# Kernel optimization log

Hardware: AMD Instinct MI355X
Metric: run time of the kernel (lower is better)

Reference implementation:

```python
import jax, jax.numpy as jnp
import numpy as np

N = 16384          # batch of signals
DIM_T = 256        # time steps per signal
DT = 0.01          # integration dt (intg_lev=1 -> dt_intg = dt)
NUF = 256          # num_units_feat
HID_XI = 128       # hidlayers_xi
HID_AUX = 64       # hidlayers_aux1_dec
LEN_INTG = DIM_T   # (dim_t-1)*intg_lev + 1 with intg_lev=1


def _linear_init(key, fan_in, fan_out):
    # torch nn.Linear default: U(-1/sqrt(fan_in), 1/sqrt(fan_in))
    s = 1.0 / np.sqrt(fan_in)
    kw, kb = jax.random.split(key)
    W = jax.random.uniform(kw, (fan_in, fan_out), minval=-s, maxval=s, dtype=jnp.float32)
    b = jax.random.uniform(kb, (fan_out,), minval=-s, maxval=s, dtype=jnp.float32)
    return W, b


def setup_inputs() -> dict:
    key = jax.random.key(0)
    ks = jax.random.split(key, 12)
    data = jax.random.normal(ks[0], (N, DIM_T), dtype=jnp.float32)
    omega = jax.random.normal(ks[1], (N, 1), dtype=jnp.float32)
    eps = jax.random.normal(ks[2], (N, 1), dtype=jnp.float32)
    # feature extractor (mlp branch): [dim_t+1 -> 256 -> 256], relu after both (actfun_output=True)
    W_feat1, b_feat1 = _linear_init(ks[3], DIM_T + 1, NUF)
    W_feat2, b_feat2 = _linear_init(ks[4], NUF, NUF)
    # xi mean head: MLP [256 -> 128 -> 1] then Softplus
    W_xim1, b_xim1 = _linear_init(ks[5], NUF, HID_XI)
    W_xim2, b_xim2 = _linear_init(ks[6], HID_XI, 1)
    # xi lnvar head: MLP [256 -> 128 -> 1]
    W_xil1, b_xil1 = _linear_init(ks[7], NUF, HID_XI)
    W_xil2, b_xil2 = _linear_init(ks[8], HID_XI, 1)
    # decoder aux1 MLP: [dim_z_aux1+1=2 -> 64 -> 1]
    W_aux1, b_aux1 = _linear_init(ks[9], 2, HID_AUX)
    W_aux2, b_aux2 = _linear_init(ks[10], HID_AUX, 1)
    return dict(data=data, omega=omega, eps=eps,
                W_feat1=W_feat1, b_feat1=b_feat1, W_feat2=W_feat2, b_feat2=b_feat2,
                W_xim1=W_xim1, b_xim1=b_xim1, W_xim2=W_xim2, b_xim2=b_xim2,
                W_xil1=W_xil1, b_xil1=b_xil1, W_xil2=W_xil2, b_xil2=b_xil2,
                W_aux1=W_aux1, b_aux1=b_aux1, W_aux2=W_aux2, b_aux2=b_aux2)


def reference(data, omega, eps,
              W_feat1, b_feat1, W_feat2, b_feat2,
              W_xim1, b_xim1, W_xim2, b_xim2,
              W_xil1, b_xil1, W_xil2, b_xil2,
              W_aux1, b_aux1, W_aux2, b_aux2):
    relu = jax.nn.relu
    # ---- encode_xi ----
    x_ = jnp.concatenate([data, omega], axis=1)                 # [n, dim_t+1]
    feat = relu(relu(x_ @ W_feat1 + b_feat1) @ W_feat2 + b_feat2)  # [n, 256]
    xi_mean = jax.nn.softplus(relu(feat @ W_xim1 + b_xim1) @ W_xim2 + b_xim2)  # [n, 1]
    xi_lnvar = relu(feat @ W_xil1 + b_xil1) @ W_xil2 + b_xil2                  # [n, 1]
    # ---- draw (reparameterization + clamp to feasible range [0, 1]) ----
    xi = xi_mean + jnp.exp(0.5 * xi_lnvar) * eps
    xi = jnp.clip(xi, 0.0, 1.0)
    # ---- decode: Euler odeint over LEN_INTG steps of state yy=[y, dy/dt] ----
    init_y = data[:, :1]                                        # [n, 1]
    initcond = jnp.concatenate([init_y, jnp.zeros_like(init_y)], axis=1)  # [n, 2]

    def step(yy, _):
        # physics: d[y, v]/dt = [v, 0]; aux MLP adds acceleration from (z_aux1=omega, y)
        aux_in = jnp.concatenate([omega, yy[:, :1]], axis=1)    # [n, 2]
        acc = relu(aux_in @ W_aux1 + b_aux1) @ W_aux2 + b_aux2  # [n, 1]
        dyy = jnp.concatenate([yy[:, 1:2], acc], axis=1)        # [n, 2]
        return yy + DT * dyy, yy

    _, yy_seq = jax.lax.scan(step, initcond, None, length=LEN_INTG)  # [len_intg, n, 2]
    y_seq = yy_seq[:, :, 0].T                                   # [n, dim_t] (intg_lev=1)
    t_intg = DT * jnp.arange(LEN_INTG, dtype=jnp.float32)       # [dim_t]
    x_PAB = jnp.exp(-jnp.abs(xi) * t_intg[None, :]) * y_seq     # [n, dim_t]
    return xi_mean, xi_lnvar, x_PAB
```

## Files before the change

kernel.cpp:

```cpp
#include <hip/hip_runtime.h>
#include <math.h>

#define NROWS 16384
#define DT_C 0.01f

typedef short s16x8 __attribute__((ext_vector_type(8)));
typedef float f32x4 __attribute__((ext_vector_type(4)));
typedef float f32x2 __attribute__((ext_vector_type(2)));
typedef unsigned long long u64;
typedef unsigned long long u64x2 __attribute__((ext_vector_type(2)));

__device__ __forceinline__ unsigned short f2bf(float f) {
    unsigned u = __float_as_uint(f);
    u += 0x7fffu + ((u >> 16) & 1u);
    return (unsigned short)(u >> 16);
}
__device__ __forceinline__ unsigned pack2bf(float a, float b) {
    return (unsigned)f2bf(a) | ((unsigned)f2bf(b) << 16);
}
template <int CTRL>
__device__ __forceinline__ float dppadd(float v) {
    int x = __builtin_amdgcn_update_dpp(0, __float_as_int(v), CTRL, 0xF, 0xF, true);
    return v + __int_as_float(x);
}
__device__ __forceinline__ float sum16(float p) {
    p = dppadd<0xB1>(p);
    p = dppadd<0x4E>(p);
    p = dppadd<0x141>(p);
    p = dppadd<0x140>(p);
    return p;
}
__device__ __forceinline__ unsigned ordf(float f) {
    unsigned u = __float_as_uint(f);
    return u ^ ((unsigned)((int)u >> 31) | 0x80000000u);
}

__global__ __launch_bounds__(256) void prep_k(
    const float* __restrict__ Wf1, const float* __restrict__ Wf2,
    const float* __restrict__ Wm1, const float* __restrict__ Wl1,
    const float* __restrict__ bm1, const float* __restrict__ bl1,
    unsigned short* __restrict__ wpack, float* __restrict__ biasH)
{
    const int id = blockIdx.x * 256 + threadIdx.x;
    const int n  = id & 255;
    const int k8 = (id >> 8) & 31;
    const int s  = id >> 13;

    unsigned short tmp[8];
    #pragma unroll
    for (int j = 0; j < 8; ++j) {
        const int k = k8 * 8 + j;
        float v;
        if (s == 0)      v = Wf1[k * 256 + n];
        else if (s == 1) v = Wf2[k * 256 + n];
        else             v = (n < 128) ? Wm1[k * 128 + n] : Wl1[k * 128 + n - 128];
        tmp[j] = f2bf(v);
    }
    *(uint4*)&wpack[((s * 32 + k8) * 256 + n) * 8] = *(const uint4*)tmp;

    if (id < 256) biasH[id] = (id < 128) ? bm1[id] : bl1[id - 128];
}

__global__ __launch_bounds__(512, 4) void fused_k(
    const float* __restrict__ data, const float* __restrict__ omega,
    const float* __restrict__ eps_g,
    const unsigned short* __restrict__ wpack, const float* __restrict__ biasH,
    const float* __restrict__ bf1, const float* __restrict__ bf2,
    const float* __restrict__ w256g,
    const float* __restrict__ Wm2, const float* __restrict__ bm2,
    const float* __restrict__ Wl2, const float* __restrict__ bl2,
    const float* __restrict__ Wa1, const float* __restrict__ ba1,
    const float* __restrict__ Wa2, const float* __restrict__ ba2,
    float* __restrict__ out_mean, float* __restrict__ out_lnvar,
    float* __restrict__ xout)
{
    __shared__ __align__(16) unsigned char smem[59136];
    unsigned short* As1 = (unsigned short*)smem;
    unsigned short* Hs  = (unsigned short*)(smem + 16384);
    float* headsF = (float*)smem;
    float* omg = (float*)(smem + 32768);
    float* xiS = omg + 32;
    float* tS  = (float*)(smem + 33024);
    float* dP  = (float*)(smem + 41728);
    u64*  keyU = (u64*)(smem + 41728);

    const int tid  = threadIdx.x;
    const int wid  = tid >> 6;
    const int lane = tid & 63;
    const int ln   = lane & 15;
    const int quad = lane >> 4;
    const int r0   = blockIdx.x * 32;

    {
        #pragma unroll
        for (int g2 = 0; g2 < 4; ++g2) {
            const int unit = g2 * 512 + tid;
            const int m    = unit >> 6;
            const int c16  = unit & 63;
            const int kblk = c16 >> 1;
            const int h    = c16 & 1;
            const float4 v = *(const float4*)&data[(size_t)(r0 + m) * 256 + c16 * 4];
            unsigned* d = (unsigned*)&As1[((kblk * 32) + (m ^ (kblk & 7))) * 8 + h * 4];
            d[0] = pack2bf(v.x, v.y);
            d[1] = pack2bf(v.z, v.w);
        }
        if (tid < 32) omg[tid] = omega[r0 + tid];
    }

    const int sr = tid >> 4;
    const int sl = tid & 15;
    float tA[4], dAv[4], dBv[4];
    u64 key[4];
    float k0f, Af, Bf, y0_s;
    {
        const float om_s = omega[r0 + sr];
        y0_s = data[(size_t)(r0 + sr) * 256];
        const u64 ky0 = ((u64)ordf(y0_s)) << 6;
        float k0p = 0.f, Ap = 0.f, Bp = 0.f;
        #pragma unroll
        for (int m = 0; m < 4; ++m) {
            const int i = sl * 4 + m;
            const float a = fmaf(om_s, Wa1[i], ba1[i]);
            const float w = Wa1[64 + i];
            const float c = Wa2[i];
            const float ca = c * a, cw = c * w;
        const bool wpos = w > 0.f;
            tA[m]  = -a / w;
            dAv[m] = wpos ? ca : -ca;
            dBv[m] = wpos ? cw : -cw;
            key[m] = (((u64)ordf(tA[m])) << 6) | (u64)i;
            const bool crossed = key[m] < ky0;
            if (wpos == crossed) { Ap += ca; Bp += cw; }
            k0p += crossed ? 1.f : 0.f;
            keyU[sr * 66 + i] = key[m];
        }
        k0f = sum16(k0p);
        Af  = sum16(Ap) + ba2[0];
        Bf  = sum16(Bp);
    }
    __syncthreads();

    {
        int rk[4] = {0, 0, 0, 0};
        const u64* krow = keyU + sr * 66;
        for (int j = 0; j < 64; j += 2) {
            const u64x2 kk = *(const u64x2*)&krow[j];
            #pragma unroll
            for (int m = 0; m < 4; ++m)
                rk[m] += (int)(kk.x < key[m]) + (int)(kk.y < key[m]);
        }
        __syncthreads();
        #pragma unroll
        for (int m = 0; m < 4; ++m) {
            const int idx = sr * 68 + 2 + rk[m];
            tS[idx] = tA[m];
            *(f32x2*)&dP[2 * idx] = f32x2{dAv[m], dBv[m]};
        }
        if (sl == 0) {
            const int b = sr * 68;
            const float INFV = __builtin_inff();
            tS[b] = -INFV; tS[b + 1] = -INFV; tS[b + 66] = INFV; tS[b + 67] = INFV;
            const f32x2 z = {0.f, 0.f};
            *(f32x2*)&dP[2 * b] = z;          *(f32x2*)&dP[2 * (b + 1)] = z;
            *(f32x2*)&dP[2 * (b + 66)] = z;   *(f32x2*)&dP[2 * (b + 67)] = z;
        }
    }

    f32x4 acc[2][2];

    auto seed = [&](const float* bias) {
        #pragma unroll
        for (int nt = 0; nt < 2; ++nt) {
            const float b = bias[wid * 32 + nt * 16 + ln];
            acc[0][nt] = f32x4{b, b, b, b};
            acc[1][nt] = acc[0][nt];
        }
    };

    auto run_stage = [&](const unsigned short* Ap, const unsigned short* wp) {
        #pragma unroll
        for (int c = 0; c < 4; ++c) {
            #pragma unroll
            for (int kk = 0; kk < 2; ++kk) {
                const int kb   = kk * 4 + quad;
                const int kblk = c * 8 + kb;
                const int f    = kblk & 7;
                s16x8 b0 = *(const s16x8*)&wp[((size_t)(kblk * 256) + wid * 32 + 0 * 16 + ln) * 8];
                s16x8 b1 = *(const s16x8*)&wp[((size_t)(kblk * 256) + wid * 32 + 1 * 16 + ln) * 8];
                s16x8 a0 = *(const s16x8*)&Ap[(kblk * 32 + (ln ^ f)) * 8];
                s16x8 a1 = *(const s16x8*)&Ap[(kblk * 32 + ((ln ^ f) + 16)) * 8];
                acc[0][0] = __builtin_amdgcn_mfma_f32_16x16x32_bf16(a0, b0, acc[0][0], 0, 0, 0);
                acc[1][0] = __builtin_amdgcn_mfma_f32_16x16x32_bf16(a1, b0, acc[1][0], 0, 0, 0);
                acc[0][1] = __builtin_amdgcn_mfma_f32_16x16x32_bf16(a0, b1, acc[0][1], 0, 0, 0);
                acc[1][1] = __builtin_amdgcn_mfma_f32_16x16x32_bf16(a1, b1, acc[1][1], 0, 0, 0);
            }
        }
    };

    auto write_packed = [&](unsigned short* dst, bool addOm) {
        #pragma unroll
        for (int nt = 0; nt < 2; ++nt) {
            const int col = wid * 32 + nt * 16 + ln;
            const int kg  = col >> 3, f = kg & 7, jj = col & 7;
            const float wo = addOm ? w256g[col] : 0.f;
            #pragma unroll
            for (int mt = 0; mt < 2; ++mt) {
                #pragma unroll
                for (int r = 0; r < 4; ++r) {
                    const int row = mt * 16 + quad * 4 + r;
                    float v = acc[mt][nt][r];
                    if (addOm) v = fmaf(omg[row], wo, v);
                    v = fmaxf(v, 0.f);
                    dst[(kg * 32 + (row ^ f)) * 8 + jj] = f2bf(v);
                }
            }
        }
    };

    seed(bf1);
    run_stage(As1, wpack);
    write_packed(Hs, true);
    __syncthreads();
    seed(bf2);
    run_stage(Hs, wpack + 65536);
    write_packed(As1, false);
    __syncthreads();
    seed(biasH);
    run_stage(As1, wpack + 131072);
    __syncthreads();
    #pragma unroll
    for (int nt = 0; nt < 2; ++nt) {
        const int col = wid * 32 + nt * 16 + ln;
        #pragma unroll
        for (int mt = 0; mt < 2; ++mt) {
            #pragma unroll
            for (int r = 0; r < 4; ++r) {
                const int row = mt * 16 + quad * 4 + r;
                headsF[row * 256 + ((col + row * 8) & 255)] = fmaxf(acc[mt][nt][r], 0.f);
            }
        }
    }
    __syncthreads();

    {
        const int m = tid >> 4, l = tid & 15;
        float pm = 0.f, pl = 0.f;
        #pragma unroll
        for (int q = 0; q < 2; ++q) {
            const int c0 = l * 8 + q * 4;
            const float4 hm = *(const float4*)&headsF[m * 256 + ((c0 + m * 8) & 255)];
            const float4 wm = *(const float4*)&Wm2[c0];
            const float4 hl = *(const float4*)&headsF[m * 256 + ((128 + c0 + m * 8) & 255)];
            const float4 wl = *(const float4*)&Wl2[c0];
            pm = fmaf(hm.w, wm.w, fmaf(hm.z, wm.z, fmaf(hm.y, wm.y, fmaf(hm.x, wm.x, pm))));
            pl = fmaf(hl.w, wl.w, fmaf(hl.z, wl.z, fmaf(hl.y, wl.y, fmaf(hl.x, wl.x, pl))));
        }
        pm = sum16(pm);
        pl = sum16(pl);
        if (l == 0) {
            const float xm  = pm + bm2[0];
            const float mean = fmaxf(xm, 0.f) + log1pf(expf(-fabsf(xm)));
            const float lnv  = pl + bl2[0];
            out_mean[r0 + m]  = mean;
            out_lnvar[r0 + m] = lnv;
            float xi = mean + expf(0.5f * lnv) * eps_g[r0 + m];
            xiS[m] = fminf(fmaxf(xi, 0.f), 1.f);
        }
    }
    __syncthreads();

    if (sl == 0) {
        const float xi   = xiS[sr];
        const float dfac = expf(-xi * DT_C);
        const float* tSr = tS + sr * 68 + 2;
        const float* dPb = dP + (sr * 68 + 2) * 2;
        int   k    = (int)k0f;
        float segA = Af, segB = Bf;
        float tLo  = tSr[k - 1], tHi = tSr[k], tHi2 = tSr[k + 1], tLo2 = tSr[k - 2];
        f32x2 dU = *(const f32x2*)&dPb[2 * k];
        f32x2 dD = *(const f32x2*)&dPb[2 * (k - 1)];
        float ym = y0_s, yc = y0_s;
        float pr = fmaf(segB, y0_s, segA);
        float d  = 1.f;
        const float DT2 = DT_C * DT_C;
        float* orow = xout + (size_t)(r0 + sr) * 256;

        auto step = [&](float& dst) {
            if (__builtin_expect(yc >= tHi, 0)) {
                do {
                    segA += dU.x; segB += dU.y;
                    dD = dU;
                    tLo2 = tLo; tLo = tHi; tHi = tHi2;
                    ++k;
                    tHi2 = tSr[k + 1];
                    dU = *(const f32x2*)&dPb[2 * k];
                } while (yc >= tHi);
            } else if (__builtin_expect(yc < tLo, 0)) {
                do {
                    segA -= dD.x; segB -= dD.y;
                    dU = dD;
                    tHi2 = tHi; tHi = tLo; tLo = tLo2;
                    --k;
                    tLo2 = tSr[k - 2];
                    dD = *(const f32x2*)&dPb[2 * (k - 1)];
                } while (yc < tLo);
            }
            const float pn = fmaf(segB, yc, segA);
            dst = ym * d;
            d *= dfac;
            const float yn = fmaf(DT2, pr, fmaf(2.f, yc, -ym));
            ym = yc; yc = yn; pr = pn;
        };

        for (int g = 0; g < 64; ++g) {
            float4 cv;
            step(cv.x); step(cv.y); step(cv.z); step(cv.w);
            *(float4*)&orow[g * 4] = cv;
        }
    }
}

extern "C" void kernel_launch(void* const* d_in, const int* in_sizes, int n_in,
                              void* d_out, int out_size, void* d_ws, size_t ws_size,
                              hipStream_t stream)
{
    const float* data    = (const float*)d_in[0];
    const float* omega   = (const float*)d_in[1];
    const float* eps     = (const float*)d_in[2];
    const float* W_feat1 = (const float*)d_in[3];
    const float* b_feat1 = (const float*)d_in[4];
    const float* W_feat2 = (const float*)d_in[5];
    const float* b_feat2 = (const float*)d_in[6];
    const float* W_xim1  = (const float*)d_in[7];
    const float* b_xim1  = (const float*)d_in[8];
    const float* W_xim2  = (const float*)d_in[9];
    const float* b_xim2  = (const float*)d_in[10];
    const float* W_xil1  = (const float*)d_in[11];
    const float* b_xil1  = (const float*)d_in[12];
    const float* W_xil2  = (const float*)d_in[13];
    const float* b_xil2  = (const float*)d_in[14];
    const float* W_aux1  = (const float*)d_in[15];
    const float* b_aux1  = (const float*)d_in[16];
    const float* W_aux2  = (const float*)d_in[17];
    const float* b_aux2  = (const float*)d_in[18];

    float* out_mean  = (float*)d_out;
    float* out_lnvar = out_mean + NROWS;
    float* out_x     = out_lnvar + NROWS;

    unsigned short* wpack = (unsigned short*)d_ws;
    float* biasH = (float*)((char*)d_ws + 3 * 32 * 256 * 8 * 2);

    prep_k<<<96, 256, 0, stream>>>(W_feat1, W_feat2, W_xim1, W_xil1,
                                   b_xim1, b_xil1, wpack, biasH);
    fused_k<<<512, 512, 0, stream>>>(data, omega, eps, wpack, biasH,
                                     b_feat1, b_feat2, W_feat1 + 256 * 256,
                                     W_xim2, b_xim2, W_xil2, b_xil2,
                                     W_aux1, b_aux1, W_aux2, b_aux2,
                                     out_mean, out_lnvar, out_x);
}
```

Before: 148.3 us.

## Consolidate serial ODE scan into one wave and preload MFMA weight fragments

The sequential Euler/segment integration used to run on one lane per 16-thread group, so all eight waves stayed resident. It now runs on 32 lanes of wave 0, and the other waves exit early, which frees SIMD slots for other blocks. Per-row initial state is staged through a small new shared-memory area instead of being held in registers across the GEMM stages. Separately, all B weight fragments for a stage are loaded into registers before the MFMA loop to hide global-load latency. The trade-offs are more branch divergence within the single integrating wave and higher register pressure, with possible spills under the 4-block launch bound.

```diff
diff --git a/kernel.cpp b/kernel.cpp
--- a/kernel.cpp
+++ b/kernel.cpp
@@ -74,7 +74,7 @@
     float* __restrict__ out_mean, float* __restrict__ out_lnvar,
     float* __restrict__ xout)
 {
-    __shared__ __align__(16) unsigned char smem[59136];
+    __shared__ __align__(16) unsigned char smem[59648];
     unsigned short* As1 = (unsigned short*)smem;
     unsigned short* Hs  = (unsigned short*)(smem + 16384);
     float* headsF = (float*)smem;
@@ -83,6 +83,7 @@
     float* tS  = (float*)(smem + 33024);
     float* dP  = (float*)(smem + 41728);
     u64*  keyU = (u64*)(smem + 41728);
+    float* initS = (float*)(smem + 59136);
 
     const int tid  = threadIdx.x;
     const int wid  = tid >> 6;
@@ -111,10 +112,9 @@
     const int sl = tid & 15;
     float tA[4], dAv[4], dBv[4];
     u64 key[4];
-    float k0f, Af, Bf, y0_s;
     {
         const float om_s = omega[r0 + sr];
-        y0_s = data[(size_t)(r0 + sr) * 256];
+        const float y0_s = data[(size_t)(r0 + sr) * 256];
         const u64 ky0 = ((u64)ordf(y0_s)) << 6;
         float k0p = 0.f, Ap = 0.f, Bp = 0.f;
         #pragma unroll
@@ -124,7 +124,7 @@
             const float w = Wa1[64 + i];
             const float c = Wa2[i];
             const float ca = c * a, cw = c * w;
-        const bool wpos = w > 0.f;
+            const bool wpos = w > 0.f;
             tA[m]  = -a / w;
             dAv[m] = wpos ? ca : -ca;
             dBv[m] = wpos ? cw : -cw;
@@ -134,9 +134,10 @@
             k0p += crossed ? 1.f : 0.f;
             keyU[sr * 66 + i] = key[m];
         }
-        k0f = sum16(k0p);
-        Af  = sum16(Ap) + ba2[0];
-        Bf  = sum16(Bp);
+        const float k0f = sum16(k0p);
+        const float Af  = sum16(Ap) + ba2[0];
+        const float Bf  = sum16(Bp);
+        if (sl == 0) *(f32x4*)&initS[sr * 4] = f32x4{y0_s, k0f, Af, Bf};
     }
     __syncthreads();
 
@@ -178,22 +179,23 @@
     };
 
     auto run_stage = [&](const unsigned short* Ap, const unsigned short* wp) {
-        #pragma unroll
-        for (int c = 0; c < 4; ++c) {
-            #pragma unroll
-            for (int kk = 0; kk < 2; ++kk) {
-                const int kb   = kk * 4 + quad;
-                const int kblk = c * 8 + kb;
-                const int f    = kblk & 7;
-                s16x8 b0 = *(const s16x8*)&wp[((size_t)(kblk * 256) + wid * 32 + 0 * 16 + ln) * 8];
-                s16x8 b1 = *(const s16x8*)&wp[((size_t)(kblk * 256) + wid * 32 + 1 * 16 + ln) * 8];
-                s16x8 a0 = *(const s16x8*)&Ap[(kblk * 32 + (ln ^ f)) * 8];
-                s16x8 a1 = *(const s16x8*)&Ap[(kblk * 32 + ((ln ^ f) + 16)) * 8];
-                acc[0][0] = __builtin_amdgcn_mfma_f32_16x16x32_bf16(a0, b0, acc[0][0], 0, 0, 0);
-                acc[1][0] = __builtin_amdgcn_mfma_f32_16x16x32_bf16(a1, b0, acc[1][0], 0, 0, 0);
-                acc[0][1] = __builtin_amdgcn_mfma_f32_16x16x32_bf16(a0, b1, acc[0][1], 0, 0, 0);
-                acc[1][1] = __builtin_amdgcn_mfma_f32_16x16x32_bf16(a1, b1, acc[1][1], 0, 0, 0);
-            }
+        s16x8 Bv0[8], Bv1[8];
+        #pragma unroll
+        for (int it = 0; it < 8; ++it) {
+            const int kblk = (it >> 1) * 8 + (it & 1) * 4 + quad;
+            Bv0[it] = *(const s16x8*)&wp[((size_t)(kblk * 256) + wid * 32 + ln) * 8];
+            Bv1[it] = *(const s16x8*)&wp[((size_t)(kblk * 256) + wid * 32 + 16 + ln) * 8];
+        }
+        #pragma unroll
+        for (int it = 0; it < 8; ++it) {
+            const int kblk = (it >> 1) * 8 + (it & 1) * 4 + quad;
+            const int f    = kblk & 7;
+            s16x8 a0 = *(const s16x8*)&Ap[(kblk * 32 + (ln ^ f)) * 8];
+            s16x8 a1 = *(const s16x8*)&Ap[(kblk * 32 + ((ln ^ f) + 16)) * 8];
+            acc[0][0] = __builtin_amdgcn_mfma_f32_16x16x32_bf16(a0, Bv0[it], acc[0][0], 0, 0, 0);
+            acc[1][0] = __builtin_amdgcn_mfma_f32_16x16x32_bf16(a1, Bv0[it], acc[1][0], 0, 0, 0);
+            acc[0][1] = __builtin_amdgcn_mfma_f32_16x16x32_bf16(a0, Bv1[it], acc[0][1], 0, 0, 0);
+            acc[1][1] = __builtin_amdgcn_mfma_f32_16x16x32_bf16(a1, Bv1[it], acc[1][1], 0, 0, 0);
         }
     };
 
@@ -269,13 +271,18 @@
     }
     __syncthreads();
 
-    if (sl == 0) {
-        const float xi   = xiS[sr];
+    if (wid != 0) return;
+    if (lane >= 32) return;
+    {
+        const int r = lane;
+        const f32x4 ini = *(const f32x4*)&initS[r * 4];
+        const float y0_s = ini.x;
+        int   k    = (int)ini.y;
+        float segA = ini.z, segB = ini.w;
+        const float xi   = xiS[r];
         const float dfac = expf(-xi * DT_C);
-        const float* tSr = tS + sr * 68 + 2;
-        const float* dPb = dP + (sr * 68 + 2) * 2;
-        int   k    = (int)k0f;
-        float segA = Af, segB = Bf;
+        const float* tSr = tS + r * 68 + 2;
+        const float* dPb = dP + (r * 68 + 2) * 2;
         float tLo  = tSr[k - 1], tHi = tSr[k], tHi2 = tSr[k + 1], tLo2 = tSr[k - 2];
         f32x2 dU = *(const f32x2*)&dPb[2 * k];
         f32x2 dD = *(const f32x2*)&dPb[2 * (k - 1)];
@@ -283,7 +290,7 @@
         float pr = fmaf(segB, y0_s, segA);
         float d  = 1.f;
         const float DT2 = DT_C * DT_C;
-        float* orow = xout + (size_t)(r0 + sr) * 256;
+        float* orow = xout + (size_t)(r0 + r) * 256;
 
         auto step = [&](float& dst) {
             if (__builtin_expect(yc >= tHi, 0)) {
```

Measured after the change: 149.2 us. About the same (+0.7%).
